# Kernel tuning notes

Hardware: AMD Instinct MI355X
Metric: run time of the kernel (lower is better)

## Reference

```python
import jax, jax.numpy as jnp
import numpy as np

B, S, D = 2, 2048, 2048
QH, KVH, HD = 32, 8, 64
GRP = QH // KVH  # GQA group size = 4


def setup_inputs() -> dict:
    key = jax.random.key(0)
    ks = jax.random.split(key, 9)
    x = jax.random.normal(ks[0], (B, S, D), jnp.float32)
    # RoPE angle table: [S, HD//2] -> stacked (cos, sin) -> [S, HD//2, 2]
    inv_freq = 1.0 / (10000.0 ** (np.arange(0, HD, 2, dtype=np.float32) / HD))
    ang = np.arange(S, dtype=np.float32)[:, None] * inv_freq[None, :]
    freqs = jnp.stack([jnp.cos(jnp.asarray(ang)), jnp.sin(jnp.asarray(ang))], axis=-1).astype(jnp.float32)
    w = 0.02
    Wq = jax.random.normal(ks[1], (D, QH * HD), jnp.float32) * w
    bq = jnp.zeros((QH * HD,), jnp.float32)
    Wk = jax.random.normal(ks[2], (D, KVH * HD), jnp.float32) * w
    bk = jnp.zeros((KVH * HD,), jnp.float32)
    Wv = jax.random.normal(ks[3], (D, KVH * HD), jnp.float32) * w
    bv = jnp.zeros((KVH * HD,), jnp.float32)
    Wo = jax.random.normal(ks[4], (QH * HD, D), jnp.float32) * w
    bo = jnp.zeros((D,), jnp.float32)
    return {"x": x, "freqs": freqs, "Wq": Wq, "bq": bq, "Wk": Wk, "bk": bk,
            "Wv": Wv, "bv": bv, "Wo": Wo, "bo": bo}


def _rope(xh, cos, sin):
    # xh: [b, s, h, hd]; complex rotation on adjacent pairs, like view_as_complex
    b, s, h, hd = xh.shape
    xp = xh.reshape(b, s, h, hd // 2, 2)
    x0, x1 = xp[..., 0], xp[..., 1]
    o0 = x0 * cos - x1 * sin
    o1 = x0 * sin + x1 * cos
    return jnp.stack([o0, o1], axis=-1).reshape(b, s, h, hd)


def reference(x, freqs, Wq, bq, Wk, bk, Wv, bv, Wo, bo):
    b, s, _ = x.shape
    q = (x @ Wq + bq).reshape(b, s, QH, HD)
    k = (x @ Wk + bk).reshape(b, s, KVH, HD)
    v = (x @ Wv + bv).reshape(b, s, KVH, HD)
    cos = freqs[:s, :, 0][None, :, None, :]  # [1, s, 1, hd//2]
    sin = freqs[:s, :, 1][None, :, None, :]
    q = _rope(q, cos, sin)
    k = _rope(k, cos, sin)
    # [b, h, s, hd]
    q = q.transpose(0, 2, 1, 3).reshape(b, KVH, GRP, s, HD)
    k = k.transpose(0, 2, 1, 3)  # [b, kvh, s, hd]
    v = v.transpose(0, 2, 1, 3)
    scores = jnp.einsum('bkgsh,bkth->bkgst', q, k) / jnp.sqrt(jnp.float32(HD))
    attn = jax.nn.softmax(scores, axis=-1)
    o = jnp.einsum('bkgst,bkth->bkgsh', attn, v)  # [b, kvh, grp, s, hd]
    o = o.reshape(b, QH, s, HD).transpose(0, 2, 1, 3).reshape(b, s, QH * HD)
    return o @ Wo + bo
```

## Files before the change

### kernel.cpp

```cpp
#include <hip/hip_runtime.h>
#include <stdint.h>

#define B_   2
#define S_   2048
#define D_   2048
#define QH_  32
#define KVH_ 8
#define HD_  64

typedef short  short8  __attribute__((ext_vector_type(8)));
typedef float  floatx4 __attribute__((ext_vector_type(4)));

__device__ __forceinline__ ushort f2b(float f) {
  union { float f; uint32_t u; } c; c.f = f;
  uint32_t u = c.u;
  return (ushort)((u + 0x7FFFu + ((u >> 16) & 1u)) >> 16);
}

__device__ __forceinline__ uint32_t fbits(float f) {
  union { float f; uint32_t u; } c; c.f = f;
  return c.u;
}

__device__ __forceinline__ short8 mk8(uint32_t a, uint32_t b, uint32_t c, uint32_t d) {
  union { uint4 u; short8 s; } v; v.u = (uint4){a, b, c, d}; return v.s;
}

__device__ __forceinline__ uint32_t cvtpk(float a, float b) {
  uint32_t r;
  asm("v_cvt_pk_bf16_f32 %0, %1, %2" : "=v"(r) : "v"(a), "v"(b));
  return r;
}

__device__ __forceinline__ void dma16(const void* g, void* l) {
  __builtin_amdgcn_global_load_lds(
      (const __attribute__((address_space(1))) uint32_t*)(uintptr_t)g,
      (__attribute__((address_space(3))) uint32_t*)(uintptr_t)l, 16, 0, 0);
}

#define QSCALE 0.18033688f


__global__ __launch_bounds__(256) void conv_x_kernel(const float* __restrict__ X,
                                                     ushort* __restrict__ Xb) {
  size_t i = ((size_t)blockIdx.x * 256 + threadIdx.x) * 4;
  float4 v = *(const float4*)(X + i);
  ushort4 o;
  o.x = f2b(v.x); o.y = f2b(v.y); o.z = f2b(v.z); o.w = f2b(v.w);
  *(ushort4*)(Xb + i) = o;
}

__global__ void tconv_all_kernel(const float* __restrict__ Wq, const float* __restrict__ Wk,
                                 const float* __restrict__ Wv, const float* __restrict__ Wo,
                                 ushort* __restrict__ wqkv, ushort* __restrict__ wo) {
  __shared__ float tile[32][33];
  int z = blockIdx.z;
  const float* W; ushort* Wt; int N;
  if (z == 0)      { W = Wq; Wt = wqkv;                        N = 2048; }
  else if (z == 1) { W = Wk; Wt = wqkv + (size_t)2048 * 2048;  N = 512;  }
  else if (z == 2) { W = Wv; Wt = wqkv + (size_t)2560 * 2048;  N = 512;  }
  else             { W = Wo; Wt = wo;                          N = 2048; }
  int bx = blockIdx.x, by = blockIdx.y;
  if (bx * 32 >= N) return;
  int tx = threadIdx.x, ty = threadIdx.y;
#pragma unroll
  for (int i = 0; i < 32; i += 8)
    tile[ty + i][tx] = W[(size_t)(by * 32 + ty + i) * N + bx * 32 + tx];
  __syncthreads();
#pragma unroll
  for (int i = 0; i < 32; i += 8)
    Wt[(size_t)(bx * 32 + ty + i) * 2048 + by * 32 + tx] = f2b(tile[tx][ty + i]);
}

__global__ void bias_kernel(const float* __restrict__ bq, const float* __restrict__ bk,
                            const float* __restrict__ bv, float* __restrict__ outb) {
  int i = blockIdx.x * 256 + threadIdx.x;
  if (i >= 3072) return;
  float v;
  if (i < 2048)      v = bq[i];
  else if (i < 2560) v = bk[i - 2048];
  else               v = bv[i - 2560];
  outb[i] = v;
}


__global__ __launch_bounds__(512, 2) void gemm_qkv_kernel(
    const ushort* __restrict__ A, const ushort* __restrict__ Bt,
    const float* __restrict__ bias, const float2* __restrict__ F2,
    ushort* __restrict__ qb, ushort* __restrict__ kb, ushort* __restrict__ vb) {
  const int K = 2048;
  __shared__ ushort sA[2][256 * 64];
  __shared__ ushort sB[2][256 * 64];
  const int tid  = threadIdx.x;
  const int bm   = blockIdx.y, bn = blockIdx.x;
  const int wave = tid >> 6, lane = tid & 63;
  const int quad = lane >> 4, l16 = lane & 15;
  const int wm2  = wave >> 2, wn4 = wave & 3;
  const int sw7  = l16 & 7;
  const int dr   = lane >> 3, du = (lane & 7) ^ dr;
  const int srow = wave * 8 + dr;
  const int lcol = (lane & 7) * 8;

  const ushort* Ab = A  + (size_t)(bm * 256) * K;
  const ushort* Bb = Bt + (size_t)(bn * 256) * K;

  floatx4 acc[8][4];
#pragma unroll
  for (int i = 0; i < 8; i++)
#pragma unroll
    for (int j = 0; j < 4; j++) acc[i][j] = (floatx4){0.f, 0.f, 0.f, 0.f};

  short8 af[4][2], bf[4][2];

#define STG_A(t, h) do {                                                      \
    dma16(Ab + (size_t)((h)*128 +      srow) * 2048 + (size_t)(t)*64 + du*8,  \
          &sA[(t)&1][((h)*128 +      srow) * 64 + lcol]);                     \
    dma16(Ab + (size_t)((h)*128 + 64 + srow) * 2048 + (size_t)(t)*64 + du*8,  \
          &sA[(t)&1][((h)*128 + 64 + srow) * 64 + lcol]);                     \
  } while (0)

#define STG_B(t, h) do {                                                      \
    dma16(Bb + (size_t)((h)*128 +      srow) * 2048 + (size_t)(t)*64 + du*8,  \
          &sB[(t)&1][((h)*128 +      srow) * 64 + lcol]);                     \
    dma16(Bb + (size_t)((h)*128 + 64 + srow) * 2048 + (size_t)(t)*64 + du*8,  \
          &sB[(t)&1][((h)*128 + 64 + srow) * 64 + lcol]);                     \
  } while (0)

#define LDA(Sb, mh) do {                                                      \
    _Pragma("unroll") for (int mi2 = 0; mi2 < 4; mi2++) {                     \
      const int rr = ((mh)*128 + wm2*64 + mi2*16 + l16) * 64;                 \
      af[mi2][0] = *(const short8*)&(Sb)[rr + (((quad    ) ^ sw7) * 8)];      \
      af[mi2][1] = *(const short8*)&(Sb)[rr + (((quad + 4) ^ sw7) * 8)];      \
    } } while (0)

#define LDB(Sb, nh) do {                                                      \
    _Pragma("unroll") for (int ni2 = 0; ni2 < 2; ni2++) {                     \
      const int rr = ((nh)*128 + wn4*32 + ni2*16 + l16) * 64;                 \
      bf[(nh)*2+ni2][0] = *(const short8*)&(Sb)[rr + (((quad    ) ^ sw7) * 8)]; \
      bf[(nh)*2+ni2][1] = *(const short8*)&(Sb)[rr + (((quad + 4) ^ sw7) * 8)]; \
    } } while (0)

#define MFMA_PH(mh, nh) do {                                                  \
    __builtin_amdgcn_s_setprio(1);                                           \
    _Pragma("unroll") for (int mi2 = 0; mi2 < 4; mi2++)                       \
    _Pragma("unroll") for (int ni2 = 0; ni2 < 2; ni2++)                       \
    _Pragma("unroll") for (int ks = 0; ks < 2; ks++)                          \
      acc[(mh)*4+mi2][(nh)*2+ni2] = __builtin_amdgcn_mfma_f32_16x16x32_bf16(  \
        af[mi2][ks], bf[(nh)*2+ni2][ks], acc[(mh)*4+mi2][(nh)*2+ni2], 0,0,0); \
    __builtin_amdgcn_s_setprio(0);                                            \
  } while (0)

#define PH_SYNC() do {                                                        \
    __builtin_amdgcn_sched_barrier(0);                                        \
    __builtin_amdgcn_s_barrier();                                             \
    asm volatile("s_waitcnt lgkmcnt(0)" ::: "memory");                        \
    __builtin_amdgcn_sched_barrier(0);                                        \
  } while (0)

#define PH_END() do {                                                         \
    __builtin_amdgcn_sched_barrier(0);                                        \
    __builtin_amdgcn_s_barrier();                                             \
    __builtin_amdgcn_sched_barrier(0);                                        \
  } while (0)

  STG_A(0, 0); STG_A(0, 1); STG_B(0, 0); STG_B(0, 1);
  STG_A(1, 0); STG_B(1, 0); STG_B(1, 1);
  asm volatile("s_waitcnt vmcnt(6)" ::: "memory");
  __builtin_amdgcn_s_barrier();

#pragma unroll 1
  for (int i = 0; i < 16; ++i) {
    const int t0 = 2 * i, t1 = 2 * i + 1;
    const bool more = (i < 15);
    const ushort* A0 = sA[0]; const ushort* B0 = sB[0];
    const ushort* A1 = sA[1]; const ushort* B1 = sB[1];

    LDB(B0, 0); LDA(A0, 0);
    STG_A(t1, 1);
    PH_SYNC(); MFMA_PH(0, 0); PH_END();

    LDB(B0, 1);
    if (more) STG_A(t0 + 2, 0);
    PH_SYNC(); MFMA_PH(0, 1); PH_END();

    LDA(A0, 1);
    if (more) STG_B(t0 + 2, 0);
    PH_SYNC(); MFMA_PH(1, 0); PH_END();

    if (more) STG_B(t0 + 2, 1);
    PH_SYNC(); MFMA_PH(1, 1);
    if (more) asm volatile("s_waitcnt vmcnt(6)" ::: "memory");
    else      asm volatile("s_waitcnt vmcnt(0)" ::: "memory");
    PH_END();

    LDB(B1, 0); LDA(A1, 0);
    if (more) STG_A(t0 + 2, 1);
    PH_SYNC(); MFMA_PH(0, 0); PH_END();

    LDB(B1, 1);
    if (more) STG_A(t1 + 2, 0);
    PH_SYNC(); MFMA_PH(0, 1); PH_END();

    LDA(A1, 1);
    if (more) STG_B(t1 + 2, 0);
    PH_SYNC(); MFMA_PH(1, 0); PH_END();

    if (more) STG_B(t1 + 2, 1);
    PH_SYNC(); MFMA_PH(1, 1);
    if (more) asm volatile("s_waitcnt vmcnt(6)" ::: "memory");
    PH_END();
  }

#undef STG_A
#undef STG_B
#undef LDA
#undef LDB
#undef MFMA_PH
#undef PH_SYNC
#undef PH_END

  const int isQ = (bn < 8);
  const int isV = (bn >= 10);
  ushort* dst = isQ ? qb : (isV ? vb : kb);
  const int NH   = isQ ? QH_ : KVH_;
  const int hoff = isQ ? 0 : (isV ? 10 : 8);
  const float sySign = (l16 & 1) ? 1.f : -1.f;
  const int dpb = l16 * 4 + (wn4 & 1) * 2;

  float bvv[4];
#pragma unroll
  for (int ni = 0; ni < 4; ni++)
    bvv[ni] = bias[bn * 256 + (ni >> 1) * 128 + wn4 * 32 + (ni & 1) * 16 + l16];

#pragma unroll
  for (int mi = 0; mi < 8; mi++) {
#pragma unroll
    for (int r = 0; r < 4; r++) {
      int row = bm * 256 + (mi >> 2) * 128 + wm2 * 64 + (mi & 3) * 16 + quad * 4 + r;
      int s = row & 2047, bb = row >> 11;
      float o[4];
      if (!isV) {
#pragma unroll
        for (int ni = 0; ni < 4; ni++) {
          float xv = acc[mi][ni][r] + bvv[ni];
          float2 cs = F2[s * 32 + (wn4 & 1) * 16 + (ni & 1) * 8 + (l16 >> 1)];
          float pp = __shfl_xor(xv, 1);
          float oo = fmaf(pp * sySign, cs.y, xv * cs.x);
          if (isQ) oo *= QSCALE;
          o[ni] = oo;
        }
      } else {
#pragma unroll
        for (int ni = 0; ni < 4; ni++) o[ni] = acc[mi][ni][r] + bvv[ni];
      }
#pragma unroll
      for (int hh = 0; hh < 2; hh++) {
        int h = (bn - hoff) * 4 + hh * 2 + (wn4 >> 1);
        size_t base = (((size_t)bb * NH + h) * S_ + s) * HD_ + dpb;
        ushort2 st; st.x = f2b(o[hh * 2 + 0]); st.y = f2b(o[hh * 2 + 1]);
        *(ushort2*)&dst[base] = st;
      }
    }
  }
}


__global__ __launch_bounds__(256) void gemm_bt_kernel(
    const ushort* __restrict__ A, const ushort* __restrict__ Bt,
    const float* __restrict__ bias, float* __restrict__ C,
    int M, int N, int K) {
  __shared__ ushort sA[2][128 * 32];
  __shared__ ushort sB[2][128 * 32];
  const int tid  = threadIdx.x;
  const int bm   = blockIdx.y, bn = blockIdx.x;
  const int wave = tid >> 6, lane = tid & 63;
  const int quad = lane >> 4, l16 = lane & 15;
  const int wm   = (wave >> 1) * 64, wn = (wave & 1) * 64;

  const ushort* Ab = A  + (size_t)(bm * 128) * K;
  const ushort* Bb = Bt + (size_t)(bn * 128) * K;

  const int gr = lane >> 2;
  const int gu = (lane & 3) * 8;

  floatx4 acc[4][4];
#pragma unroll
  for (int i = 0; i < 4; i++)
#pragma unroll
    for (int j = 0; j < 4; j++) acc[i][j] = (floatx4){0.f, 0.f, 0.f, 0.f};

#pragma unroll
  for (int j = 0; j < 2; j++) {
    int row = j * 64 + wave * 16 + gr;
    dma16(Ab + (size_t)row * K + gu, &sA[0][j * 2048 + wave * 512]);
    dma16(Bb + (size_t)row * K + gu, &sB[0][j * 2048 + wave * 512]);
  }

  int cur = 0;
  for (int k0 = 0; k0 < K; k0 += 32) {
    __syncthreads();
    if (k0 + 32 < K) {
      int nxt = cur ^ 1;
#pragma unroll
      for (int j = 0; j < 2; j++) {
        int row = j * 64 + wave * 16 + gr;
        dma16(Ab + (size_t)row * K + k0 + 32 + gu, &sA[nxt][j * 2048 + wave * 512]);
        dma16(Bb + (size_t)row * K + k0 + 32 + gu, &sB[nxt][j * 2048 + wave * 512]);
      }
    }
    short8 af[4], bf[4];
#pragma unroll
    for (int mi = 0; mi < 4; mi++)
      af[mi] = *(const short8*)&sA[cur][(wm + mi * 16 + l16) * 32 + quad * 8];
#pragma unroll
    for (int ni = 0; ni < 4; ni++)
      bf[ni] = *(const short8*)&sB[cur][(wn + ni * 16 + l16) * 32 + quad * 8];
#pragma unroll
    for (int mi = 0; mi < 4; mi++)
#pragma unroll
      for (int ni = 0; ni < 4; ni++)
        acc[mi][ni] = __builtin_amdgcn_mfma_f32_16x16x32_bf16(
            af[mi], bf[ni], acc[mi][ni], 0, 0, 0);
    cur ^= 1;
  }

#pragma unroll
  for (int mi = 0; mi < 4; mi++) {
#pragma unroll
    for (int ni = 0; ni < 4; ni++) {
      int col  = bn * 128 + wn + ni * 16 + l16;
      float bv = bias[col];
#pragma unroll
      for (int r = 0; r < 4; r++) {
        int row = bm * 128 + wm + mi * 16 + quad * 4 + r;
        C[(size_t)row * N + col] = acc[mi][ni][r] + bv;
      }
    }
  }
}


__global__ void vpack_kernel(const ushort* __restrict__ vb, ushort* __restrict__ Vt) {
  __shared__ ushort tile[64][65];
  int s0 = blockIdx.x * 64;
  int bh = blockIdx.y;
  int tx = threadIdx.x, ty = threadIdx.y;
  int pc = (tx & 32) | ((tx & 12) << 1) | ((tx & 16) >> 2) | (tx & 3);
#pragma unroll
  for (int i = 0; i < 64; i += 8)
    tile[ty + i][tx] = vb[((size_t)bh * S_ + s0 + ty + i) * HD_ + tx];
  __syncthreads();
#pragma unroll
  for (int i = 0; i < 64; i += 8) {
    int dp = ty + i;
    int dt = (dp & 3) * 16 + (dp >> 2);
    Vt[((size_t)bh * HD_ + dt) * S_ + s0 + pc] = tile[tx][dp];
  }
}


__global__ __launch_bounds__(512, 4) void attn_kernel(
    const ushort* __restrict__ Q, const ushort* __restrict__ K,
    const ushort* __restrict__ Vt, ushort* __restrict__ O) {
  const int id  = blockIdx.x + 8 * (blockIdx.y + 32 * blockIdx.z);
  const int kvh = id & 7;
  const int qt  = (id >> 3) & 7;
  const int qh  = kvh * 4 + ((id >> 6) & 3);
  const int b   = id >> 8;
  const int tid = threadIdx.x;
  const int wave = tid >> 6, lane = tid & 63;
  const int quad = lane >> 4, l16 = lane & 15;

  __shared__ ushort kBuf[2][64 * 64];
  __shared__ ushort vBuf[2][64 * 64];

  const ushort* Qh = Q  + ((size_t)(b * QH_ + qh)) * S_ * HD_;
  const ushort* Kh = K  + ((size_t)(b * KVH_ + kvh)) * S_ * HD_;
  const ushort* Vh = Vt + ((size_t)(b * KVH_ + kvh)) * HD_ * S_;

  const int dr = lane >> 3;
  const int du = (lane & 7) ^ (dr & 7);
  const size_t kLaneOff = (size_t)(wave * 8 + dr) * 64 + du * 8;
  const size_t vLaneOff = (size_t)(wave * 8 + dr) * S_ + du * 8;
  const int swz = l16 & 7;

  const int q0 = qt * 256 + wave * 32;
  short8 aq[2][2];
#pragma unroll
  for (int m = 0; m < 2; m++)
#pragma unroll
    for (int s2 = 0; s2 < 2; s2++)
      aq[m][s2] = *(const short8*)(Qh + (size_t)(q0 + m * 16 + l16) * HD_ + s2 * 32 + quad * 8);

  floatx4 oacc[2][4];
#pragma unroll
  for (int m = 0; m < 2; m++)
#pragma unroll
    for (int t = 0; t < 4; t++) oacc[m][t] = (floatx4){0.f, 0.f, 0.f, 0.f};
  float ls[2] = {0.f, 0.f};

  dma16(Kh + kLaneOff, &kBuf[0][wave * 512]);
  dma16(Vh + vLaneOff, &vBuf[0][wave * 512]);

  int cur = 0;
  for (int kv0 = 0; kv0 < S_; kv0 += 64) {
    __syncthreads();
    if (kv0 + 64 < S_) {
      int nxt = cur ^ 1;
      dma16(Kh + (size_t)(kv0 + 64) * 64 + kLaneOff, &kBuf[nxt][wave * 512]);
      dma16(Vh + (size_t)(kv0 + 64) + vLaneOff,      &vBuf[nxt][wave * 512]);
    }

#pragma unroll
    for (int u = 0; u < 2; u++) {
      uint32_t pk[2][4];
#pragma unroll
      for (int cc = 0; cc < 2; cc++) {
        const int c = u * 2 + cc;
        short8 kf0 = *(const short8*)&kBuf[cur][(c * 16 + l16) * 64 + ((quad ^ swz) * 8)];
        short8 kf1 = *(const short8*)&kBuf[cur][(c * 16 + l16) * 64 + (((4 + quad) ^ swz) * 8)];
#pragma unroll
        for (int m = 0; m < 2; m++) {
          floatx4 sc = (floatx4){0.f, 0.f, 0.f, 0.f};
          __builtin_amdgcn_s_setprio(1);
          sc = __builtin_amdgcn_mfma_f32_16x16x32_bf16(kf0, aq[m][0], sc, 0, 0, 0);
          sc = __builtin_amdgcn_mfma_f32_16x16x32_bf16(kf1, aq[m][1], sc, 0, 0, 0);
          __builtin_amdgcn_s_setprio(0);
          float p0 = __builtin_amdgcn_exp2f(sc[0]);
          float p1 = __builtin_amdgcn_exp2f(sc[1]);
          float p2 = __builtin_amdgcn_exp2f(sc[2]);
          float p3 = __builtin_amdgcn_exp2f(sc[3]);
          ls[m] += (p0 + p1) + (p2 + p3);
          pk[m][cc * 2 + 0] = cvtpk(p0, p1);
          pk[m][cc * 2 + 1] = cvtpk(p2, p3);
        }
      }
#pragma unroll
      for (int t = 0; t < 4; t++) {
        const int row = (t * 16 + l16) * 64;
        short8 vf = *(const short8*)&vBuf[cur][row + (((u * 4 + quad) ^ swz) * 8)];
        __builtin_amdgcn_s_setprio(1);
#pragma unroll
        for (int m = 0; m < 2; m++) {
          short8 ap = mk8(pk[m][0], pk[m][1], pk[m][2], pk[m][3]);
          oacc[m][t] = __builtin_amdgcn_mfma_f32_16x16x32_bf16(ap, vf, oacc[m][t], 0, 0, 0);
        }
        __builtin_amdgcn_s_setprio(0);
      }
    }
    cur ^= 1;
  }

#pragma unroll
  for (int m = 0; m < 2; m++) {
    ls[m] += __shfl_xor(ls[m], 16);
    ls[m] += __shfl_xor(ls[m], 32);
  }
#pragma unroll
  for (int m = 0; m < 2; m++) {
#pragma unroll
    for (int r = 0; r < 4; r++) {
      float l = __shfl(ls[m], (lane & 48) | (quad * 4 + r));
      float inv = 1.0f / l;
      int srow = q0 + m * 16 + quad * 4 + r;
      size_t base = ((size_t)b * S_ + srow) * (QH_ * HD_) + (size_t)qh * HD_;
#pragma unroll
      for (int t = 0; t < 4; t++)
        O[base + t * 16 + l16] = f2b(oacc[m][t][r] * inv);
    }
  }
}


extern "C" void kernel_launch(void* const* d_in, const int* in_sizes, int n_in,
                              void* d_out, int out_size, void* d_ws, size_t ws_size,
                              hipStream_t stream) {
  const float* x  = (const float*)d_in[0];
  const float* fr = (const float*)d_in[1];
  const float* Wq = (const float*)d_in[2];
  const float* bq = (const float*)d_in[3];
  const float* Wk = (const float*)d_in[4];
  const float* bk = (const float*)d_in[5];
  const float* Wv = (const float*)d_in[6];
  const float* bv = (const float*)d_in[7];
  const float* Wo = (const float*)d_in[8];
  const float* bo = (const float*)d_in[9];
  float* out = (float*)d_out;
  char* ws = (char*)d_ws;

  ushort* xb    = (ushort*)(ws + 0);
  ushort* wqkv  = (ushort*)(ws + 16777216);
  ushort* wo    = (ushort*)(ws + 29360128);
  float*  biasq = (float* )(ws + 37748736);
  ushort* qb    = (ushort*)(ws + 37761024);
  ushort* kb    = (ushort*)(ws + 54538240);
  ushort* vb    = (ushort*)(ws + 58732544);
  ushort* vt    = (ushort*)(ws + 62926848);
  ushort* ob    = xb;

  conv_x_kernel<<<8192, 256, 0, stream>>>(x, xb);
  tconv_all_kernel<<<dim3(64, 64, 4), dim3(32, 8), 0, stream>>>(Wq, Wk, Wv, Wo, wqkv, wo);
  bias_kernel<<<12, 256, 0, stream>>>(bq, bk, bv, biasq);

  gemm_qkv_kernel<<<dim3(3072 / 256, 4096 / 256), 512, 0, stream>>>(
      xb, wqkv, biasq, (const float2*)fr, qb, kb, vb);

  vpack_kernel<<<dim3(2048 / 64, 16), dim3(64, 8), 0, stream>>>(vb, vt);

  attn_kernel<<<dim3(8, 32, 2), 512, 0, stream>>>(qb, kb, vt, ob);

  gemm_bt_kernel<<<dim3(2048 / 128, 4096 / 128), 256, 0, stream>>>(
      ob, wo, bo, out, 4096, 2048, 2048);
}
```

Measured before the change: 309.6 us.

## Fuse V transpose-pack and bias gathering into QKV GEMM epilogue

The QKV GEMM epilogue now writes V directly in the permuted transposed layout the attention kernel reads, so the separate vpack kernel and the intermediate V buffer go away. Bias values are read straight from bq/bk/bv, which drops the small bias concatenation kernel. This saves two launches and one round trip of V through global memory. In exchange the V stores are scattered 8-byte writes with a large stride, and the new index mapping has to reproduce the old permutation exactly.

Result: faster. 296.3 us (-4.3%).

```diff
diff --git a/kernel.cpp b/kernel.cpp
--- a/kernel.cpp
+++ b/kernel.cpp
@@ -72,23 +72,12 @@
     Wt[(size_t)(bx * 32 + ty + i) * 2048 + by * 32 + tx] = f2b(tile[tx][ty + i]);
 }
 
-__global__ void bias_kernel(const float* __restrict__ bq, const float* __restrict__ bk,
-                            const float* __restrict__ bv, float* __restrict__ outb) {
-  int i = blockIdx.x * 256 + threadIdx.x;
-  if (i >= 3072) return;
-  float v;
-  if (i < 2048)      v = bq[i];
-  else if (i < 2560) v = bk[i - 2048];
-  else               v = bv[i - 2560];
-  outb[i] = v;
-}
-
 
 __global__ __launch_bounds__(512, 2) void gemm_qkv_kernel(
     const ushort* __restrict__ A, const ushort* __restrict__ Bt,
-    const float* __restrict__ bias, const float2* __restrict__ F2,
-    ushort* __restrict__ qb, ushort* __restrict__ kb, ushort* __restrict__ vb) {
-  const int K = 2048;
+    const float* __restrict__ bq, const float* __restrict__ bk,
+    const float* __restrict__ bv, const float2* __restrict__ F2,
+    ushort* __restrict__ qb, ushort* __restrict__ kb, ushort* __restrict__ vt) {
   __shared__ ushort sA[2][256 * 64];
   __shared__ ushort sB[2][256 * 64];
   const int tid  = threadIdx.x;
@@ -101,8 +90,8 @@
   const int srow = wave * 8 + dr;
   const int lcol = (lane & 7) * 8;
 
-  const ushort* Ab = A  + (size_t)(bm * 256) * K;
-  const ushort* Bb = Bt + (size_t)(bn * 256) * K;
+  const ushort* Ab = A  + (size_t)(bm * 256) * 2048;
+  const ushort* Bb = Bt + (size_t)(bn * 256) * 2048;
 
   floatx4 acc[8][4];
 #pragma unroll
@@ -221,25 +210,28 @@
 
   const int isQ = (bn < 8);
   const int isV = (bn >= 10);
-  ushort* dst = isQ ? qb : (isV ? vb : kb);
-  const int NH   = isQ ? QH_ : KVH_;
-  const int hoff = isQ ? 0 : (isV ? 10 : 8);
   const float sySign = (l16 & 1) ? 1.f : -1.f;
-  const int dpb = l16 * 4 + (wn4 & 1) * 2;
+
+  const float* bsrc = isQ ? bq : (isV ? bv : bk);
+  const int    boff = isQ ? 0  : (isV ? 2560 : 2048);
 
   float bvv[4];
 #pragma unroll
   for (int ni = 0; ni < 4; ni++)
-    bvv[ni] = bias[bn * 256 + (ni >> 1) * 128 + wn4 * 32 + (ni & 1) * 16 + l16];
-
-#pragma unroll
-  for (int mi = 0; mi < 8; mi++) {
-#pragma unroll
-    for (int r = 0; r < 4; r++) {
-      int row = bm * 256 + (mi >> 2) * 128 + wm2 * 64 + (mi & 3) * 16 + quad * 4 + r;
-      int s = row & 2047, bb = row >> 11;
-      float o[4];
-      if (!isV) {
+    bvv[ni] = bsrc[bn * 256 + (ni >> 1) * 128 + wn4 * 32 + (ni & 1) * 16 + l16 - boff];
+
+  if (!isV) {
+    ushort* dst = isQ ? qb : kb;
+    const int NH   = isQ ? QH_ : KVH_;
+    const int hoff = isQ ? 0 : 8;
+    const int dpb  = l16 * 4 + (wn4 & 1) * 2;
+#pragma unroll
+    for (int mi = 0; mi < 8; mi++) {
+#pragma unroll
+      for (int r = 0; r < 4; r++) {
+        int row = bm * 256 + (mi >> 2) * 128 + wm2 * 64 + (mi & 3) * 16 + quad * 4 + r;
+        int s = row & 2047, bb = row >> 11;
+        float o[4];
 #pragma unroll
         for (int ni = 0; ni < 4; ni++) {
           float xv = acc[mi][ni][r] + bvv[ni];
@@ -249,16 +241,31 @@
           if (isQ) oo *= QSCALE;
           o[ni] = oo;
         }
-      } else {
-#pragma unroll
-        for (int ni = 0; ni < 4; ni++) o[ni] = acc[mi][ni][r] + bvv[ni];
-      }
-#pragma unroll
-      for (int hh = 0; hh < 2; hh++) {
-        int h = (bn - hoff) * 4 + hh * 2 + (wn4 >> 1);
-        size_t base = (((size_t)bb * NH + h) * S_ + s) * HD_ + dpb;
-        ushort2 st; st.x = f2b(o[hh * 2 + 0]); st.y = f2b(o[hh * 2 + 1]);
-        *(ushort2*)&dst[base] = st;
+#pragma unroll
+        for (int hh = 0; hh < 2; hh++) {
+          int h = (bn - hoff) * 4 + hh * 2 + (wn4 >> 1);
+          size_t base = (((size_t)bb * NH + h) * S_ + s) * HD_ + dpb;
+          ushort2 st; st.x = f2b(o[hh * 2 + 0]); st.y = f2b(o[hh * 2 + 1]);
+          *(ushort2*)&dst[base] = st;
+        }
+      }
+    }
+  } else {
+#pragma unroll
+    for (int mi = 0; mi < 8; mi++) {
+      int row0 = bm * 256 + (mi >> 2) * 128 + wm2 * 64 + (mi & 3) * 16 + quad * 4;
+      int bb   = row0 >> 11;
+      int posb = ((row0 & 2047) & ~63) + (mi & 2) * 16 + quad * 8 + (mi & 1) * 4;
+#pragma unroll
+      for (int ni = 0; ni < 4; ni++) {
+        int h  = (bn - 10) * 4 + (ni >> 1) * 2 + (wn4 >> 1);
+        int dt = (wn4 & 1) * 32 + (ni & 1) * 16 + l16;
+        ushort4 st;
+        st.x = f2b(acc[mi][ni][0] + bvv[ni]);
+        st.y = f2b(acc[mi][ni][1] + bvv[ni]);
+        st.z = f2b(acc[mi][ni][2] + bvv[ni]);
+        st.w = f2b(acc[mi][ni][3] + bvv[ni]);
+        *(ushort4*)&vt[(((size_t)bb * 8 + h) * 64 + dt) * (size_t)S_ + posb] = st;
       }
     }
   }
@@ -336,25 +343,6 @@
         C[(size_t)row * N + col] = acc[mi][ni][r] + bv;
       }
     }
-  }
-}
-
-
-__global__ void vpack_kernel(const ushort* __restrict__ vb, ushort* __restrict__ Vt) {
-  __shared__ ushort tile[64][65];
-  int s0 = blockIdx.x * 64;
-  int bh = blockIdx.y;
-  int tx = threadIdx.x, ty = threadIdx.y;
-  int pc = (tx & 32) | ((tx & 12) << 1) | ((tx & 16) >> 2) | (tx & 3);
-#pragma unroll
-  for (int i = 0; i < 64; i += 8)
-    tile[ty + i][tx] = vb[((size_t)bh * S_ + s0 + ty + i) * HD_ + tx];
-  __syncthreads();
-#pragma unroll
-  for (int i = 0; i < 64; i += 8) {
-    int dp = ty + i;
-    int dt = (dp & 3) * 16 + (dp >> 2);
-    Vt[((size_t)bh * HD_ + dt) * S_ + s0 + pc] = tile[tx][dp];
   }
 }
 
@@ -491,21 +479,16 @@
   ushort* xb    = (ushort*)(ws + 0);
   ushort* wqkv  = (ushort*)(ws + 16777216);
   ushort* wo    = (ushort*)(ws + 29360128);
-  float*  biasq = (float* )(ws + 37748736);
   ushort* qb    = (ushort*)(ws + 37761024);
   ushort* kb    = (ushort*)(ws + 54538240);
-  ushort* vb    = (ushort*)(ws + 58732544);
   ushort* vt    = (ushort*)(ws + 62926848);
   ushort* ob    = xb;
 
   conv_x_kernel<<<8192, 256, 0, stream>>>(x, xb);
   tconv_all_kernel<<<dim3(64, 64, 4), dim3(32, 8), 0, stream>>>(Wq, Wk, Wv, Wo, wqkv, wo);
-  bias_kernel<<<12, 256, 0, stream>>>(bq, bk, bv, biasq);
 
   gemm_qkv_kernel<<<dim3(3072 / 256, 4096 / 256), 512, 0, stream>>>(
-      xb, wqkv, biasq, (const float2*)fr, qb, kb, vb);
-
-  vpack_kernel<<<dim3(2048 / 64, 16), dim3(64, 8), 0, stream>>>(vb, vt);
+      xb, wqkv, bq, bk, bv, (const float2*)fr, qb, kb, vt);
 
   attn_kernel<<<dim3(8, 32, 2), 512, 0, stream>>>(qb, kb, vt, ob);
 
```
